# Performance work log

Hardware: AMD Instinct MI355X
Metric: run time of the kernel (lower is better)

## Reference

```python
import jax, jax.numpy as jnp
import numpy as np

B, C, H, W, R = 8, 256, 64, 64, 16


def setup_inputs() -> dict:
    key = jax.random.key(0)
    ks = jax.random.split(key, 14)
    def w(k, shape, fan):
        return (jax.random.normal(k, shape, jnp.float32) / np.sqrt(fan)).astype(jnp.float32)
    return {
        "features_depth": jax.random.normal(ks[0], (B, C, H, W), jnp.float32),
        "features_semseg": jax.random.normal(ks[1], (B, C, H, W), jnp.float32),
        "W0": w(ks[2], (C, 2 * C), 2 * C),          # conv_split0 1x1, [out,in]
        "Wdw": w(ks[3], (C, 1, 3, 3), 9),            # depthwise 3x3, groups=C
        "Wq": w(ks[4], (C, C), C),                   # Linear weights [out,in]
        "Wk": w(ks[5], (C, C), C),
        "Wv": w(ks[6], (C, C), C),
        "Wp": w(ks[7], (C, C), C),
        "bp": jnp.zeros((C,), jnp.float32),
        "Wsplit": w(ks[8], (C, C), C),               # conv_split 1x1
        "se_d_w1": w(ks[9], (C // R, C), C),         # SE squeeze conv1x1 (depth)
        "se_d_w2": w(ks[10], (C, C // R), C // R),
        "se_s_w1": w(ks[11], (C // R, C), C),        # SE squeeze conv1x1 (semseg)
        "se_s_w2": w(ks[12], (C, C // R), C // R),
    }


def _l2norm(a, eps=1e-12):
    n = jnp.linalg.norm(a, axis=-1, keepdims=True)
    return a / jnp.maximum(n, eps)


def _se(x, w1, w2):
    # x: [B,C,H,W]; global avg pool -> 1x1 convs -> sigmoid gate
    p = x.mean(axis=(2, 3))                                  # [B,C]
    h = jax.nn.relu(jnp.einsum('rc,bc->br', w1, p))          # [B,C/R]
    g = jax.nn.sigmoid(jnp.einsum('cr,br->bc', w2, h))       # [B,C]
    return x * g[:, :, None, None]


def reference(features_depth, features_semseg, W0, Wdw, Wq, Wk, Wv, Wp, bp,
              Wsplit, se_d_w1, se_d_w2, se_s_w1, se_s_w2):
    x = jnp.concatenate([features_depth, features_semseg], axis=1)  # [B,2C,H,W]
    x = jnp.einsum('oc,bchw->bohw', W0, x)                          # 1x1 conv
    x = jax.lax.conv_general_dilated(
        x, Wdw, window_strides=(1, 1), padding='SAME',
        dimension_numbers=('NCHW', 'OIHW', 'NCHW'), feature_group_count=C)
    xt = x.transpose(0, 2, 3, 1).reshape(B, H * W, C)               # [B,N,C]
    q = (xt @ Wq.T).transpose(0, 2, 1)                              # [B,C,N]
    k = (xt @ Wk.T).transpose(0, 2, 1)
    v = (xt @ Wv.T).transpose(0, 2, 1)
    q = _l2norm(q)
    k = _l2norm(k)
    attn = jax.nn.softmax(jnp.einsum('bcn,bdn->bcd', k, q), axis=-1)  # [B,C,C]
    y = jnp.einsum('bcd,bdn->bcn', attn, v)                         # [B,C,N]
    y = y.transpose(0, 2, 1)                                        # [B,N,C]
    y = y @ Wp.T + bp                                               # proj
    out_c = y.reshape(B, H, W, C).transpose(0, 3, 1, 2)             # [B,C,H,W]
    out_c = jnp.einsum('oc,bchw->bohw', Wsplit, out_c)              # 1x1 conv
    out_depth = _se(out_c, se_d_w1, se_d_w2) + features_depth
    out_semseg = _se(out_c, se_s_w1, se_s_w2) + features_semseg
    return (out_depth, out_semseg)
```

## Files before the change

### kernel.cpp

```cpp
#include <hip/hip_runtime.h>
#include <cstdint>

#define DEVI __device__ __forceinline__

using fx4 = __attribute__((ext_vector_type(4))) float;
using bf8 = __attribute__((ext_vector_type(8))) __bf16;
using s8v = __attribute__((ext_vector_type(8))) short;
using s4v = __attribute__((ext_vector_type(4))) short;
typedef unsigned short u16;
typedef unsigned int u32;

DEVI float b2f(u16 u) { return __builtin_bit_cast(float, (u32)u << 16); }
DEVI u16 f2b(float f) {
  u32 u = __builtin_bit_cast(u32, f);
  return (u16)((u + 0x7fffu + ((u >> 16) & 1u)) >> 16);
}

#define GLOAD(g, l)                                                          \
  __builtin_amdgcn_global_load_lds(                                          \
      (const __attribute__((address_space(1))) unsigned int*)(g),            \
      (__attribute__((address_space(3))) unsigned int*)(l), 16, 0, 0)

__global__ __launch_bounds__(256) void prep(const float* __restrict__ W0,
                                            const float* __restrict__ Wq,
                                            const float* __restrict__ Wk,
                                            const float* __restrict__ Wv,
                                            const float* __restrict__ Wsp,
                                            const float* __restrict__ Wp,
                                            const float* __restrict__ bp,
                                            u16* __restrict__ w0b,
                                            u16* __restrict__ wqk2,
                                            u16* __restrict__ wvtb,
                                            u16* __restrict__ wcb,
                                            float* __restrict__ bcb) {
  __shared__ float row[256];
  __shared__ float red[4];
  const int y = blockIdx.y;
  const int t = threadIdx.x;
  if (y == 0) {
    const int i = blockIdx.x * 256 + t;
    if (i < 131072) w0b[i] = f2b(W0[i]);
  } else if (y == 1) {
    const int i = blockIdx.x * 256 + t;
    if (i < 262144) {
      const int r = i >> 9, c = i & 511;
      const float* src = (r < 256) ? Wq : Wk;
      wqk2[i] = f2b(src[((r & 255) << 8) + (c & 255)]);
    }
  } else if (y == 2) {
    const int i = blockIdx.x * 256 + t;
    if (i < 65536) {
      const int e = i >> 8, d = i & 255;
      wvtb[i] = f2b(Wv[d * 256 + e]);
    }
  } else {
    if (blockIdx.x >= 256) return;
    const int o = blockIdx.x;
    row[t] = Wsp[o * 256 + t];
    __syncthreads();
    float acc = 0.f;
    for (int c = 0; c < 256; ++c) acc += row[c] * Wp[c * 256 + t];
    wcb[o * 256 + t] = f2b(acc);
    float pb = row[t] * bp[t];
#pragma unroll
    for (int m = 32; m > 0; m >>= 1) pb += __shfl_xor(pb, m);
    if ((t & 63) == 0) red[t >> 6] = pb;
    __syncthreads();
    if (t == 0) bcb[o] = red[0] + red[1] + red[2] + red[3];
  }
}

__global__ __launch_bounds__(512) void conv0f(const float* __restrict__ fd,
                                              const float* __restrict__ fs,
                                              const u16* __restrict__ w0b,
                                              u16* __restrict__ x0) {
  __shared__ u16 tmp[64 * 132];
  __shared__ u16 ldsA[128 * 64];
  __shared__ u16 ldsB[256 * 64];
  const int b = blockIdx.y;
  const int bm = blockIdx.x * 128;
  const int t = threadIdx.x;
  const int wid = t >> 6, lane = t & 63;
  const int wm = wid >> 2, wn = wid & 3;
  fx4 acc[4][4] = {};
  for (int kt = 0; kt < 512; kt += 64) {
#pragma unroll
    for (int i = 0; i < 4; ++i) {
      const int r = i * 64 + (t >> 3);
      const int kq = (t & 7) ^ (r & 7);
      GLOAD(w0b + (long)r * 512 + kt + kq * 8, &ldsB[i * 4096 + wid * 512]);
    }
    const float* src = ((kt < 256) ? fd : fs) + ((long)b * 256 + (kt & 255)) * 4096L + bm;
#pragma unroll
    for (int p = 0; p < 4; ++p) {
      const int c = (t >> 5) + p * 16;
      const int n4 = (t & 31) * 4;
      const fx4 v = *(const fx4*)&src[(long)c * 4096 + n4];
      s4v pk;
#pragma unroll
      for (int j = 0; j < 4; ++j) pk[j] = (short)f2b(v[j]);
      *(s4v*)&tmp[c * 132 + n4] = pk;
    }
    __syncthreads();
#pragma unroll
    for (int pass = 0; pass < 2; ++pass) {
      const int n = t & 127;
      const int g = (t >> 7) + pass * 4;
      s8v pk;
#pragma unroll
      for (int j = 0; j < 8; ++j) pk[j] = (short)tmp[(g * 8 + j) * 132 + n];
      *(s8v*)&ldsA[n * 64 + ((g ^ (n & 7)) * 8)] = pk;
    }
    __syncthreads();
#pragma unroll
    for (int ko = 0; ko < 2; ++ko) {
      bf8 af[4], bfr[4];
      const int kq = ko * 4 + (lane >> 4);
#pragma unroll
      for (int f = 0; f < 4; ++f) {
        const int ar = wm * 64 + f * 16 + (lane & 15);
        af[f] = *(const bf8*)&ldsA[ar * 64 + ((kq ^ (ar & 7)) * 8)];
        const int br = wn * 64 + f * 16 + (lane & 15);
        bfr[f] = *(const bf8*)&ldsB[br * 64 + ((kq ^ (br & 7)) * 8)];
      }
#pragma unroll
      for (int fm = 0; fm < 4; ++fm)
#pragma unroll
        for (int fn = 0; fn < 4; ++fn)
          acc[fm][fn] = __builtin_amdgcn_mfma_f32_16x16x32_bf16(af[fm], bfr[fn], acc[fm][fn], 0, 0, 0);
    }
    __syncthreads();
  }
#pragma unroll
  for (int fm = 0; fm < 4; ++fm) {
    const int m0 = wm * 64 + fm * 16 + ((lane >> 4) << 2);
#pragma unroll
    for (int fn = 0; fn < 4; ++fn) {
      const int o = wn * 64 + fn * 16 + (lane & 15);
#pragma unroll
      for (int r = 0; r < 4; ++r)
        x0[((long)b << 20) + (long)(bm + m0 + r) * 256 + o] = f2b(acc[fm][fn][r]);
    }
  }
}

template <typename OT, int BIAS, int EPI>
__global__ __launch_bounds__(256) void gemm_nt(
    const u16* __restrict__ A, long sA, int lda,
    const u16* __restrict__ B, long sB, int ldb,
    OT* __restrict__ C, long sC, long sCs, int ldc,
    const float* __restrict__ bias, int Keff, int ksplit,
    const float* __restrict__ wqf, const float* __restrict__ wkf,
    float* __restrict__ dpart, float* __restrict__ poolpart) {
  __shared__ u16 ldsA[128 * 64];
  __shared__ u16 ldsB[128 * 64];
  const int z = blockIdx.z;
  const int bb = z / ksplit;
  const int ss = z - bb * ksplit;
  const int bm = blockIdx.x * 128;
  const int bn = blockIdx.y * 128;
  const u16* Ab = A + bb * sA + (long)ss * Keff + (long)bm * lda;
  const u16* Bb = B + bb * sB + (long)ss * Keff + (long)bn * ldb;
  const int tid = threadIdx.x;
  const int wid = tid >> 6;
  const int lane = tid & 63;
  const int wm = wid >> 1, wn = wid & 1;
  const int srow = tid >> 3;
  const int slot = tid & 7;

  fx4 acc[4][4] = {};
  for (int kt = 0; kt < Keff; kt += 64) {
#pragma unroll
    for (int i = 0; i < 4; ++i) {
      const int row = i * 32 + srow;
      const int kq = slot ^ (row & 7);
      GLOAD(Ab + (long)row * lda + kt + kq * 8, &ldsA[i * 2048 + wid * 512]);
      GLOAD(Bb + (long)row * ldb + kt + kq * 8, &ldsB[i * 2048 + wid * 512]);
    }
    __syncthreads();
#pragma unroll
    for (int ko = 0; ko < 2; ++ko) {
      bf8 af[4], bfr[4];
      const int kq = ko * 4 + (lane >> 4);
#pragma unroll
      for (int f = 0; f < 4; ++f) {
        const int ar = wm * 64 + f * 16 + (lane & 15);
        af[f] = *(const bf8*)&ldsA[ar * 64 + ((kq ^ (ar & 7)) * 8)];
        const int br = wn * 64 + f * 16 + (lane & 15);
        bfr[f] = *(const bf8*)&ldsB[br * 64 + ((kq ^ (br & 7)) * 8)];
      }
#pragma unroll
      for (int fm = 0; fm < 4; ++fm)
#pragma unroll
        for (int fn = 0; fn < 4; ++fn)
          acc[fm][fn] = __builtin_amdgcn_mfma_f32_16x16x32_bf16(af[fm], bfr[fn], acc[fm][fn], 0, 0, 0);
    }
    __syncthreads();
  }
  if constexpr (EPI == 1) {
    u16* S2b = (u16*)C + bb * sC;
    float dp[4][4];
#pragma unroll
    for (int fm = 0; fm < 4; ++fm)
#pragma unroll
      for (int r = 0; r < 4; ++r) dp[fm][r] = 0.f;
#pragma unroll
    for (int fm = 0; fm < 4; ++fm) {
      const int m0 = bm + wm * 64 + fm * 16 + ((lane >> 4) << 2);
#pragma unroll
      for (int fn = 0; fn < 4; ++fn) {
        const int n0 = bn + wn * 64 + fn * 16 + (lane & 15);
#pragma unroll
        for (int r = 0; r < 4; ++r) {
          const float v = acc[fm][fn][r];
          const int m = m0 + r;
          if (m < 256) {
            const u16 hi = f2b(v);
            S2b[(long)m * 512 + n0] = hi;
            S2b[(long)m * 512 + 256 + n0] = f2b(v - b2f(hi));
          }
          const float* wr = (m < 256) ? (wqf + (long)m * 256) : (wkf + (long)(m - 256) * 256);
          dp[fm][r] += v * wr[n0];
        }
      }
    }
#pragma unroll
    for (int fm = 0; fm < 4; ++fm)
#pragma unroll
      for (int r = 0; r < 4; ++r) {
        float s = dp[fm][r];
        s += __shfl_xor(s, 1); s += __shfl_xor(s, 2);
        s += __shfl_xor(s, 4); s += __shfl_xor(s, 8);
        if ((lane & 15) == 0) {
          const int m = bm + wm * 64 + fm * 16 + ((lane >> 4) << 2) + r;
          dpart[(long)(blockIdx.y * 2 + wn) * 4096 + bb * 512 + m] = s;
        }
      }
    return;
  }
  if constexpr (EPI == 4) {
    float* odp = (float*)C + bb * sC;
    float* osp = (float*)C + 8388608 + bb * sC;
    const float* fdp = wqf + bb * sC;
    const float* fsp = wkf + bb * sC;
#pragma unroll
    for (int fm = 0; fm < 4; ++fm) {
      const int m0 = bm + wm * 64 + fm * 16 + ((lane >> 4) << 2);
#pragma unroll
      for (int r = 0; r < 4; ++r) {
        const int m = m0 + r;
        const float bv = bias[m];
        const float g1 = dpart[bb * 256 + m];
        const float g2 = poolpart[bb * 256 + m];
        const long rowb = (long)m * ldc;
#pragma unroll
        for (int fn = 0; fn < 4; ++fn) {
          const int n0 = bn + wn * 64 + fn * 16 + (lane & 15);
          const float v = acc[fm][fn][r] + bv;
          odp[rowb + n0] = v * g1 + fdp[rowb + n0];
          osp[rowb + n0] = v * g2 + fsp[rowb + n0];
        }
      }
    }
    return;
  }
  OT* Cb = C + bb * sC + ss * sCs;
#pragma unroll
  for (int fm = 0; fm < 4; ++fm) {
    const int m0 = bm + wm * 64 + fm * 16 + ((lane >> 4) << 2);
#pragma unroll
    for (int fn = 0; fn < 4; ++fn) {
      const int n0 = bn + wn * 64 + fn * 16 + (lane & 15);
#pragma unroll
      for (int r = 0; r < 4; ++r) {
        float v = acc[fm][fn][r];
        if (BIAS == 2) v += bias[m0 + r];
        if constexpr (sizeof(OT) == 2) Cb[(long)(m0 + r) * ldc + n0] = (OT)f2b(v);
        else Cb[(long)(m0 + r) * ldc + n0] = v;
      }
    }
  }
}

__global__ __launch_bounds__(256) void dwconv3x3(const u16* __restrict__ x,
                                                 const float* __restrict__ wdw,
                                                 u16* __restrict__ y) {
  __shared__ float w[9][256];
  const int t = threadIdx.x;
  for (int i = t; i < 2304; i += 256) w[i % 9][i / 9] = wdw[i];
  __syncthreads();
  const int nb = blockIdx.x;
  const int b = nb >> 9;
  const int n0 = (nb & 511) << 3;
  const int tn = t >> 5;
  const int tc = (t & 31) << 3;
  const int n = n0 + tn;
  const int hh = n >> 6, ww2 = n & 63;
  const u16* base = x + ((long)b << 20);
  float acc[8] = {0.f, 0.f, 0.f, 0.f, 0.f, 0.f, 0.f, 0.f};
#pragma unroll
  for (int ky = 0; ky < 3; ++ky) {
    const int hy = hh + ky - 1;
    if ((unsigned)hy >= 64u) continue;
#pragma unroll
    for (int kx = 0; kx < 3; ++kx) {
      const int wx = ww2 + kx - 1;
      if ((unsigned)wx >= 64u) continue;
      const s8v v = *(const s8v*)&base[(((hy << 6) + wx) << 8) + tc];
      const int kk = ky * 3 + kx;
      const fx4 wa = *(const fx4*)&w[kk][tc];
      const fx4 wb = *(const fx4*)&w[kk][tc + 4];
#pragma unroll
      for (int j = 0; j < 4; ++j) {
        acc[j] += wa[j] * b2f((u16)v[j]);
        acc[4 + j] += wb[j] * b2f((u16)v[4 + j]);
      }
    }
  }
  s8v o;
#pragma unroll
  for (int j = 0; j < 8; ++j) o[j] = (short)f2b(acc[j]);
  *(s8v*)&y[((long)b << 20) + ((long)n << 8) + tc] = o;
}

__global__ void btrans2(const u16* __restrict__ x, u16* __restrict__ y,
                        float* __restrict__ cspart) {
  __shared__ u16 t[32][34];
  __shared__ float ps[8][32];
  const int b = blockIdx.z;
  const int n0 = blockIdx.x * 32;
  const int c0 = blockIdx.y * 32;
  const int tx = threadIdx.x, ty = threadIdx.y;
  const u16* sp = x + (long)b * 1048576 + (long)n0 * 256 + c0;
  float cs = 0.f;
#pragma unroll
  for (int j = 0; j < 4; ++j) {
    int i = ty + j * 8;
    const u16 v = sp[(long)i * 256 + tx];
    t[i][tx] = v;
    cs += b2f(v);
  }
  ps[ty][tx] = cs;
  __syncthreads();
  u16* op = y + (long)b * 1048576 + (long)c0 * 4096 + n0;
#pragma unroll
  for (int j = 0; j < 4; ++j) {
    int r = ty + j * 8;
    op[(long)r * 4096 + tx] = t[tx][r];
  }
  if (ty == 0) {
    float s = 0.f;
#pragma unroll
    for (int k = 0; k < 8; ++k) s += ps[k][tx];
    cspart[(long)blockIdx.x * 2048 + b * 256 + c0 + tx] = s;
  }
}

__global__ __launch_bounds__(256) void gsplit(const float* __restrict__ part,
                                              u16* __restrict__ G2) {
  const int i4 = (blockIdx.x * 256 + threadIdx.x) * 4;
  fx4 s = {0.f, 0.f, 0.f, 0.f};
#pragma unroll
  for (int ss = 0; ss < 8; ++ss) s += *(const fx4*)(part + (long)ss * 524288 + i4);
  const int b = i4 >> 16, rem = i4 & 65535, e = rem >> 8, c0 = rem & 255;
  u16* d = G2 + (long)b * 131072 + (long)e * 512 + c0;
  s4v hi, lo;
#pragma unroll
  for (int j = 0; j < 4; ++j) {
    u16 h = f2b(s[j]);
    hi[j] = (short)h;
    lo[j] = (short)f2b(s[j] - b2f(h));
  }
  *(s4v*)d = hi;
  *(s4v*)(d + 256) = lo;
}

__global__ __launch_bounds__(256) void softmax_g2(const float* __restrict__ araw,
                                                  const float* __restrict__ dpart,
                                                  u16* __restrict__ out) {
  const int wid = threadIdx.x >> 6, lane = threadIdx.x & 63;
  const int t = threadIdx.x;
  const int b = blockIdx.x >> 6;
  __shared__ float rq[256];
  float dq = dpart[b * 512 + t] + dpart[4096 + b * 512 + t] +
             dpart[8192 + b * 512 + t] + dpart[12288 + b * 512 + t];
  rq[t] = 1.f / fmaxf(sqrtf(fmaxf(dq, 0.f)), 1e-12f);
  __syncthreads();
  const long row = (long)blockIdx.x * 4 + wid;
  const int c = (int)(row & 255);
  const int ki = b * 512 + 256 + c;
  float dk = dpart[ki] + dpart[4096 + ki] + dpart[8192 + ki] + dpart[12288 + ki];
  const float rk = 1.f / fmaxf(sqrtf(fmaxf(dk, 0.f)), 1e-12f);
  fx4 v = ((const fx4*)(araw + row * 256))[lane];
  v[0] *= rk * rq[lane * 4];     v[1] *= rk * rq[lane * 4 + 1];
  v[2] *= rk * rq[lane * 4 + 2]; v[3] *= rk * rq[lane * 4 + 3];
  float m = fmaxf(fmaxf(v[0], v[1]), fmaxf(v[2], v[3]));
#pragma unroll
  for (int o = 32; o > 0; o >>= 1) m = fmaxf(m, __shfl_xor(m, o));
  float e0 = __expf(v[0] - m), e1 = __expf(v[1] - m);
  float e2 = __expf(v[2] - m), e3 = __expf(v[3] - m);
  float s4 = e0 + e1 + e2 + e3;
#pragma unroll
  for (int o = 32; o > 0; o >>= 1) s4 += __shfl_xor(s4, o);
  const float inv = 1.f / s4;
  u16* op = out + row * 256 + lane * 4;
  op[0] = f2b(e0 * inv); op[1] = f2b(e1 * inv);
  op[2] = f2b(e2 * inv); op[3] = f2b(e3 * inv);
}

__global__ __launch_bounds__(256) void mwfuse(const u16* __restrict__ attnb,
                                              const u16* __restrict__ wvtb,
                                              const u16* __restrict__ wcb,
                                              u16* __restrict__ wfin) {
  __shared__ u16 lds[25088];
  const int M1OFF = 0;
  const int A2OFF = 16896;
  const int B1OFF = 0;
  const int A1OFF = 16384;
  const int e0 = blockIdx.x * 64;
  const int b = blockIdx.y;
  const int t = threadIdx.x;
  const int wid = t >> 6, lane = t & 63;
  const int srow = t >> 3, slot = t & 7;
  const u16* attn = attnb + (long)b * 65536;

  fx4 acc[4][4] = {};
  for (int kt = 0; kt < 256; kt += 64) {
#pragma unroll
    for (int i = 0; i < 8; ++i) {
      const int row = i * 32 + srow;
      const int kq = slot ^ (row & 7);
      GLOAD(attn + (long)row * 256 + kt + kq * 8, &lds[B1OFF + i * 2048 + wid * 512]);
    }
#pragma unroll
    for (int i = 0; i < 2; ++i) {
      const int row = i * 32 + srow;
      const int kq = slot ^ (row & 7);
      GLOAD(wvtb + (long)(e0 + row) * 256 + kt + kq * 8, &lds[A1OFF + i * 2048 + wid * 512]);
    }
    __syncthreads();
#pragma unroll
    for (int ko = 0; ko < 2; ++ko) {
      bf8 af[4], bfr[4];
      const int kq = ko * 4 + (lane >> 4);
#pragma unroll
      for (int f = 0; f < 4; ++f) {
        const int ar = f * 16 + (lane & 15);
        af[f] = *(const bf8*)&lds[A1OFF + ar * 64 + ((kq ^ (ar & 7)) * 8)];
        const int br = wid * 64 + f * 16 + (lane & 15);
        bfr[f] = *(const bf8*)&lds[B1OFF + br * 64 + ((kq ^ (br & 7)) * 8)];
      }
#pragma unroll
      for (int fm = 0; fm < 4; ++fm)
#pragma unroll
        for (int fn = 0; fn < 4; ++fn)
          acc[fm][fn] = __builtin_amdgcn_mfma_f32_16x16x32_bf16(af[fm], bfr[fn], acc[fm][fn], 0, 0, 0);
    }
    __syncthreads();
  }
#pragma unroll
  for (int fm = 0; fm < 4; ++fm) {
    const int ep0 = fm * 16 + ((lane >> 4) << 2);
#pragma unroll
    for (int fn = 0; fn < 4; ++fn) {
      const int c = wid * 64 + fn * 16 + (lane & 15);
#pragma unroll
      for (int r = 0; r < 4; ++r)
        lds[M1OFF + (ep0 + r) * 264 + c] = f2b(acc[fm][fn][r]);
    }
  }
  __syncthreads();
  fx4 acc2[4][4] = {};
  for (int kt = 0; kt < 256; kt += 32) {
#pragma unroll
    for (int i = 0; i < 4; ++i) {
      const int row = i * 64 + (t >> 2);
      const int kq = (t & 3) ^ (row & 3);
      GLOAD(wcb + (long)row * 256 + kt + kq * 8, &lds[A2OFF + i * 2048 + wid * 512]);
    }
    __syncthreads();
    bf8 af[4], bfr[4];
    const int kq = lane >> 4;
#pragma unroll
    for (int f = 0; f < 4; ++f) {
      const int ar = wid * 64 + f * 16 + (lane & 15);
      af[f] = *(const bf8*)&lds[A2OFF + ar * 32 + ((kq ^ (ar & 3)) * 8)];
      const int br = f * 16 + (lane & 15);
      bfr[f] = *(const bf8*)&lds[M1OFF + br * 264 + kt + kq * 8];
    }
#pragma unroll
    for (int fm = 0; fm < 4; ++fm)
#pragma unroll
      for (int fn = 0; fn < 4; ++fn)
        acc2[fm][fn] = __builtin_amdgcn_mfma_f32_16x16x32_bf16(af[fm], bfr[fn], acc2[fm][fn], 0, 0, 0);
    __syncthreads();
  }
  u16* wf = wfin + (long)b * 65536;
#pragma unroll
  for (int fm = 0; fm < 4; ++fm) {
    const int o0 = wid * 64 + fm * 16 + ((lane >> 4) << 2);
#pragma unroll
    for (int fn = 0; fn < 4; ++fn) {
      const int e = e0 + fn * 16 + (lane & 15);
#pragma unroll
      for (int r = 0; r < 4; ++r)
        wf[(long)(o0 + r) * 256 + e] = f2b(acc2[fm][fn][r]);
    }
  }
}

__global__ __launch_bounds__(256) void sefuse(const float* __restrict__ cspart,
                                              const u16* __restrict__ wfin,
                                              const float* __restrict__ bcb,
                                              const float* __restrict__ w1d, const float* __restrict__ w2d,
                                              const float* __restrict__ w1s, const float* __restrict__ w2s,
                                              float* __restrict__ gd, float* __restrict__ gs) {
  const int b = blockIdx.x;
  const int t = threadIdx.x;
  __shared__ float xm[256], p[256], hd[16], hs[16];
  float s = 0.f;
#pragma unroll 8
  for (int sl = 0; sl < 128; ++sl) s += cspart[(long)sl * 2048 + b * 256 + t];
  xm[t] = s;
  __syncthreads();
  const u16* wf = wfin + (long)b * 65536 + (long)t * 256;
  float acc = 0.f;
#pragma unroll 4
  for (int e = 0; e < 256; e += 8) {
    const s8v w8 = *(const s8v*)&wf[e];
    const fx4 x0v = *(const fx4*)&xm[e];
    const fx4 x1v = *(const fx4*)&xm[e + 4];
#pragma unroll
    for (int j = 0; j < 4; ++j) {
      acc += b2f((u16)w8[j]) * x0v[j];
      acc += b2f((u16)w8[4 + j]) * x1v[j];
    }
  }
  p[t] = acc * (1.f / 4096.f) + bcb[t];
  __syncthreads();
  if (t < 16) {
    float ad = 0.f, as2 = 0.f;
    for (int j = 0; j < 256; ++j) {
      ad += w1d[t * 256 + j] * p[j];
      as2 += w1s[t * 256 + j] * p[j];
    }
    hd[t] = fmaxf(ad, 0.f);
    hs[t] = fmaxf(as2, 0.f);
  }
  __syncthreads();
  float ad = 0.f, as2 = 0.f;
#pragma unroll
  for (int r = 0; r < 16; ++r) {
    ad += w2d[t * 16 + r] * hd[r];
    as2 += w2s[t * 16 + r] * hs[r];
  }
  gd[b * 256 + t] = 1.f / (1.f + __expf(-ad));
  gs[b * 256 + t] = 1.f / (1.f + __expf(-as2));
}

extern "C" void kernel_launch(void* const* d_in, const int* in_sizes, int n_in,
                              void* d_out, int out_size, void* d_ws, size_t ws_size,
                              hipStream_t stream) {
  const float* fd  = (const float*)d_in[0];
  const float* fs  = (const float*)d_in[1];
  const float* W0  = (const float*)d_in[2];
  const float* Wdw = (const float*)d_in[3];
  const float* Wq  = (const float*)d_in[4];
  const float* Wk  = (const float*)d_in[5];
  const float* Wv  = (const float*)d_in[6];
  const float* Wp  = (const float*)d_in[7];
  const float* bp  = (const float*)d_in[8];
  const float* Wsp = (const float*)d_in[9];
  const float* w1d = (const float*)d_in[10];
  const float* w2d = (const float*)d_in[11];
  const float* w1s = (const float*)d_in[12];
  const float* w2s = (const float*)d_in[13];

  char* ws = (char*)d_ws;
  u16* x0b    = (u16*)(ws + 0);
  u16* xtb    = (u16*)(ws + 16777216);
  u16* xtT    = (u16*)(ws + 33554432);
  float* part = (float*)(ws + 50331648);
  u16* G2     = (u16*)(ws + 67108864);
  u16* S2     = (u16*)(ws + 69206016);
  float* araw = (float*)(ws + 71303168);
  u16* attnb  = (u16*)(ws + 73400320);
  u16* wfin   = (u16*)(ws + 74448896);
  u16* w0b    = (u16*)(ws + 75497472);
  u16* wqk2   = (u16*)(ws + 75759616);
  u16* wvtb   = (u16*)(ws + 76283904);
  u16* wcb    = (u16*)(ws + 76414976);
  float* bcb  = (float*)(ws + 76546048);
  float* dpart = (float*)(ws + 76547072);
  float* cspart = (float*)(ws + 76611584);
  float* gdp  = (float*)(ws + 77660160);
  float* gsp  = (float*)(ws + 77668352);
  float* od   = (float*)d_out;

  prep<<<dim3(2048, 4), 256, 0, stream>>>(W0, Wq, Wk, Wv, Wsp, Wp, bp,
                                          w0b, wqk2, wvtb, wcb, bcb);
  conv0f<<<dim3(32, 8), 512, 0, stream>>>(fd, fs, w0b, x0b);
  dwconv3x3<<<4096, 256, 0, stream>>>(x0b, Wdw, xtb);
  btrans2<<<dim3(128, 8, 8), dim3(32, 8), 0, stream>>>(xtb, xtT, cspart);
  gemm_nt<float, 0, 0><<<dim3(2, 2, 64), 256, 0, stream>>>(
      xtT, 1048576, 4096, xtT, 1048576, 4096,
      part, 65536, 524288, 256, nullptr, 512, 8, nullptr, nullptr, nullptr, nullptr);
  gsplit<<<512, 256, 0, stream>>>(part, G2);
  gemm_nt<u16, 0, 1><<<dim3(4, 2, 8), 256, 0, stream>>>(
      wqk2, 0, 512, G2, 131072, 512, S2, 131072, 0, 512, nullptr, 512, 1,
      Wq, Wk, dpart, nullptr);
  gemm_nt<float, 0, 0><<<dim3(2, 2, 8), 256, 0, stream>>>(
      wqk2 + 131072, 0, 512, S2, 131072, 512, araw, 65536, 0, 256, nullptr, 512, 1,
      nullptr, nullptr, nullptr, nullptr);
  softmax_g2<<<512, 256, 0, stream>>>(araw, dpart, attnb);
  mwfuse<<<dim3(4, 8), 256, 0, stream>>>(attnb, wvtb, wcb, wfin);
  sefuse<<<8, 256, 0, stream>>>(cspart, wfin, bcb, w1d, w2d, w1s, w2s, gdp, gsp);
  gemm_nt<float, 0, 4><<<dim3(2, 32, 8), 256, 0, stream>>>(
      wfin, 65536, 256, xtb, 1048576, 256, od, 1048576, 0, 4096, bcb, 256, 1,
      fd, fs, gdp, gsp);
}
```

Baseline: 168.7 us.

## Fuse depthwise conv with transpose and channel-sum into one kernel

```diff
diff --git a/kernel.cpp b/kernel.cpp
--- a/kernel.cpp
+++ b/kernel.cpp
@@ -282,77 +282,75 @@
   }
 }
 
-__global__ __launch_bounds__(256) void dwconv3x3(const u16* __restrict__ x,
-                                                 const float* __restrict__ wdw,
-                                                 u16* __restrict__ y) {
+__global__ __launch_bounds__(256) void dwconvT(const u16* __restrict__ x,
+                                               const float* __restrict__ wdw,
+                                               u16* __restrict__ y,
+                                               u16* __restrict__ yT,
+                                               float* __restrict__ cspart) {
   __shared__ float w[9][256];
+  __shared__ u16 tb2[32][264];
+  __shared__ float psf[8][256];
   const int t = threadIdx.x;
   for (int i = t; i < 2304; i += 256) w[i % 9][i / 9] = wdw[i];
+  const int b = blockIdx.x >> 7;
+  const int strip = blockIdx.x & 127;
+  const int n0 = strip * 32;
+  const int h = n0 >> 6;
+  const int w0 = n0 & 63;
+  const int tc = (t & 31) * 8;
+  const int tn = t >> 5;
+  const u16* base = x + ((long)b << 20);
+  float csl[8] = {0.f, 0.f, 0.f, 0.f, 0.f, 0.f, 0.f, 0.f};
   __syncthreads();
-  const int nb = blockIdx.x;
-  const int b = nb >> 9;
-  const int n0 = (nb & 511) << 3;
-  const int tn = t >> 5;
-  const int tc = (t & 31) << 3;
-  const int n = n0 + tn;
-  const int hh = n >> 6, ww2 = n & 63;
-  const u16* base = x + ((long)b << 20);
-  float acc[8] = {0.f, 0.f, 0.f, 0.f, 0.f, 0.f, 0.f, 0.f};
-#pragma unroll
-  for (int ky = 0; ky < 3; ++ky) {
-    const int hy = hh + ky - 1;
-    if ((unsigned)hy >= 64u) continue;
-#pragma unroll
-    for (int kx = 0; kx < 3; ++kx) {
-      const int wx = ww2 + kx - 1;
-      if ((unsigned)wx >= 64u) continue;
-      const s8v v = *(const s8v*)&base[(((hy << 6) + wx) << 8) + tc];
-      const int kk = ky * 3 + kx;
-      const fx4 wa = *(const fx4*)&w[kk][tc];
-      const fx4 wb = *(const fx4*)&w[kk][tc + 4];
-#pragma unroll
-      for (int j = 0; j < 4; ++j) {
-        acc[j] += wa[j] * b2f((u16)v[j]);
-        acc[4 + j] += wb[j] * b2f((u16)v[4 + j]);
-      }
-    }
-  }
-  s8v o;
-#pragma unroll
-  for (int j = 0; j < 8; ++j) o[j] = (short)f2b(acc[j]);
-  *(s8v*)&y[((long)b << 20) + ((long)n << 8) + tc] = o;
-}
-
-__global__ void btrans2(const u16* __restrict__ x, u16* __restrict__ y,
-                        float* __restrict__ cspart) {
-  __shared__ u16 t[32][34];
-  __shared__ float ps[8][32];
-  const int b = blockIdx.z;
-  const int n0 = blockIdx.x * 32;
-  const int c0 = blockIdx.y * 32;
-  const int tx = threadIdx.x, ty = threadIdx.y;
-  const u16* sp = x + (long)b * 1048576 + (long)n0 * 256 + c0;
-  float cs = 0.f;
-#pragma unroll
-  for (int j = 0; j < 4; ++j) {
-    int i = ty + j * 8;
-    const u16 v = sp[(long)i * 256 + tx];
-    t[i][tx] = v;
-    cs += b2f(v);
-  }
-  ps[ty][tx] = cs;
+#pragma unroll
+  for (int p = 0; p < 4; ++p) {
+    const int nn = p * 8 + tn;
+    const int ww = w0 + nn;
+    float acc[8] = {0.f, 0.f, 0.f, 0.f, 0.f, 0.f, 0.f, 0.f};
+#pragma unroll
+    for (int ky = 0; ky < 3; ++ky) {
+      const int hy = h + ky - 1;
+      if ((unsigned)hy >= 64u) continue;
+#pragma unroll
+      for (int kx = 0; kx < 3; ++kx) {
+        const int wx = ww + kx - 1;
+        if ((unsigned)wx >= 64u) continue;
+        const s8v v = *(const s8v*)&base[(((hy << 6) + wx) << 8) + tc];
+        const int kk = ky * 3 + kx;
+        const fx4 wa = *(const fx4*)&w[kk][tc];
+        const fx4 wb = *(const fx4*)&w[kk][tc + 4];
+#pragma unroll
+        for (int j = 0; j < 4; ++j) {
+          acc[j] += wa[j] * b2f((u16)v[j]);
+          acc[4 + j] += wb[j] * b2f((u16)v[4 + j]);
+        }
+      }
+    }
+    s8v o;
+#pragma unroll
+    for (int j = 0; j < 8; ++j) {
+      o[j] = (short)f2b(acc[j]);
+      csl[j] += b2f((u16)o[j]);
+    }
+    *(s8v*)&y[((long)b << 20) + (long)((n0 + nn) << 8) + tc] = o;
+    *(s8v*)&tb2[nn][tc] = o;
+  }
+#pragma unroll
+  for (int j = 0; j < 8; ++j) psf[tn][tc + j] = csl[j];
   __syncthreads();
-  u16* op = y + (long)b * 1048576 + (long)c0 * 4096 + n0;
-#pragma unroll
-  for (int j = 0; j < 4; ++j) {
-    int r = ty + j * 8;
-    op[(long)r * 4096 + tx] = t[tx][r];
-  }
-  if (ty == 0) {
+  const int cg = t >> 5;
+  const int nn2 = t & 31;
+  u16* yb = yT + ((long)b << 20);
+#pragma unroll
+  for (int cb = 0; cb < 256; cb += 8) {
+    const int c = cb + cg;
+    yb[(long)c * 4096 + n0 + nn2] = tb2[nn2][c];
+  }
+  if (t < 256) {
     float s = 0.f;
 #pragma unroll
-    for (int k = 0; k < 8; ++k) s += ps[k][tx];
-    cspart[(long)blockIdx.x * 2048 + b * 256 + c0 + tx] = s;
+    for (int k = 0; k < 8; ++k) s += psf[k][t];
+    cspart[(long)strip * 2048 + b * 256 + t] = s;
   }
 }
 
@@ -600,8 +598,7 @@
   prep<<<dim3(2048, 4), 256, 0, stream>>>(W0, Wq, Wk, Wv, Wsp, Wp, bp,
                                           w0b, wqk2, wvtb, wcb, bcb);
   conv0f<<<dim3(32, 8), 512, 0, stream>>>(fd, fs, w0b, x0b);
-  dwconv3x3<<<4096, 256, 0, stream>>>(x0b, Wdw, xtb);
-  btrans2<<<dim3(128, 8, 8), dim3(32, 8), 0, stream>>>(xtb, xtT, cspart);
+  dwconvT<<<1024, 256, 0, stream>>>(x0b, Wdw, xtb, xtT, cspart);
   gemm_nt<float, 0, 0><<<dim3(2, 2, 64), 256, 0, stream>>>(
       xtT, 1048576, 4096, xtT, 1048576, 4096,
       part, 65536, 524288, 256, nullptr, 512, 8, nullptr, nullptr, nullptr, nullptr);
```

Measured after the change: 165.8 us. About the same (-1.7%).
